# Performance work log

Hardware: AMD Instinct MI355X
Metric: run time of the kernel (lower is better)

## Reference

```python
import jax, jax.numpy as jnp
import numpy as np

N = 262144        # BS(16) * MAX_FRAMES(256) * num_joints(64), flattened
D_IN = 4          # IN_FEAT: (x, y, z, conf) per joint
D_OUT = 512       # OUT_FEAT
NUM_JOINTS = 64   # embedding vocab size
PAD_FRAC = 0.1


def _uniform(key, shape, fan_in):
    s = 1.0 / np.sqrt(fan_in)
    return jax.random.uniform(key, shape, jnp.float32, minval=-s, maxval=s)


def setup_inputs() -> dict:
    key = jax.random.key(0)
    ks = jax.random.split(key, 12)
    joint_info = jax.random.normal(ks[0], (N, D_IN), jnp.float32)
    pad = jax.random.uniform(ks[1], (N,)) < PAD_FRAC
    joint_info = jnp.where(pad[:, None], 0.0, joint_info)  # all-zero rows = padding
    joint_token = jax.random.randint(ks[2], (N,), 0, NUM_JOINTS)
    emb = jax.random.normal(ks[3], (NUM_JOINTS, D_OUT), jnp.float32)
    W1 = _uniform(ks[4], (D_OUT // 4, D_IN), D_IN)
    b1 = _uniform(ks[5], (D_OUT // 4,), D_IN)
    W2 = _uniform(ks[6], (D_OUT // 2, D_OUT // 4), D_OUT // 4)
    b2 = _uniform(ks[7], (D_OUT // 2,), D_OUT // 4)
    W3 = _uniform(ks[8], (D_OUT // 4, D_OUT // 2), D_OUT // 2)
    b3 = _uniform(ks[9], (D_OUT // 4,), D_OUT // 2)
    W4 = _uniform(ks[10], (D_OUT, D_OUT // 4), D_OUT // 4)  # last layer: no bias
    return {"joint_info": joint_info, "joint_token": joint_token, "emb": emb,
            "W1": W1, "b1": b1, "W2": W2, "b2": b2, "W3": W3, "b3": b3, "W4": W4}


def _mlp(x, layers):
    # residual when in/out widths match; GELU (exact, like torch nn.GELU) except after last layer
    out = x
    n = len(layers)
    for i, (W, b) in enumerate(layers):
        y = out @ W.T
        if b is not None:
            y = y + b
        out = y + out if y.shape[-1] == out.shape[-1] else y
        if i != n - 1:
            out = jax.nn.gelu(out, approximate=False)
    return out


def reference(joint_info, joint_token, emb, W1, b1, W2, b2, W3, b3, W4):
    layers = [(W1, b1), (W2, b2), (W3, b3), (W4, None)]
    out = _mlp(joint_info, layers)                 # [N, D_OUT]
    out = out + emb[joint_token]                   # embedding add for non-pad path
    pad_mask = jnp.all(joint_info == 0, axis=-1)   # [N]
    # pad rows get embedding(0); non-pad rows get MLP output + token embedding
    return jnp.where(pad_mask[:, None], emb[0], out)
```

## Files before the change

kernel.cpp:

```cpp
#include <hip/hip_runtime.h>
#include <math.h>


typedef float  f32x4  __attribute__((ext_vector_type(4)));
typedef short  s16x8  __attribute__((ext_vector_type(8)));
typedef __bf16 bf16x8 __attribute__((ext_vector_type(8)));

__device__ __forceinline__ unsigned short f2bf(float x) {
  unsigned u = __builtin_bit_cast(unsigned, x);
  u = (u + 0x7FFFu + ((u >> 16) & 1u)) >> 16;
  return (unsigned short)u;
}
__device__ __forceinline__ float gelu_exact(float x) {
  return 0.5f * x * (1.0f + erff(x * 0.70710678118654752f));
}

__global__ void embed_prep(const float* __restrict__ W2, const float* __restrict__ W3,
                           const float* __restrict__ W4, short* __restrict__ ws) {
  int tid = blockIdx.x * 256 + threadIdx.x;
  const float* W; int K; int base; int e;
  if (tid < 4096)      { W = W2; K = 128; base = 0;     e = tid; }
  else if (tid < 8192) { W = W3; K = 256; base = 32768; e = tid - 4096; }
  else                 { W = W4; K = 128; base = 65536; e = tid - 8192; }
  int lane = e & 63, f = e >> 6;
  int kt = K >> 5;
  int nn = f / kt, kk = f - nn * kt;
  int n  = nn * 16 + (lane & 15);
  int k0 = kk * 32 + (lane >> 4) * 8;
  const float* src = W + n * K + k0;
  s16x8 v;
#pragma unroll
  for (int j = 0; j < 8; j++) v[j] = (short)f2bf(src[j]);
  *reinterpret_cast<s16x8*>(ws + base + e * 8) = v;
}

__global__ __launch_bounds__(256) void embed_main(
    const float* __restrict__ jinfo, const int* __restrict__ jtok,
    const float* __restrict__ emb,   const float* __restrict__ W1,
    const float* __restrict__ b1,    const float* __restrict__ b2,
    const float* __restrict__ b3,    const short* __restrict__ wsW,
    float* __restrict__ out) {
  __shared__ short lds_act[4][8192];
  const int lane = threadIdx.x & 63;
  const int wave = threadIdx.x >> 6;
  const int q = lane >> 4, c = lane & 15;
  const int rowBase = blockIdx.x * 128 + wave * 32;
  short* S = lds_act[wave];

  const float4* jp = reinterpret_cast<const float4*>(jinfo);

  float4 x0 = jp[rowBase + c];
  float4 x1 = jp[rowBase + 16 + c];
  s16x8 a2s[2][4];
#pragma unroll
  for (int kk = 0; kk < 4; kk++) {
#pragma unroll
    for (int j = 0; j < 8; j++) {
      int f = kk * 32 + q * 8 + j;
      float4 w = reinterpret_cast<const float4*>(W1)[f];
      float bb = b1[f];
      float h0 = fmaf(w.x, x0.x, fmaf(w.y, x0.y, fmaf(w.z, x0.z, fmaf(w.w, x0.w, bb))));
      float h1 = fmaf(w.x, x1.x, fmaf(w.y, x1.y, fmaf(w.z, x1.z, fmaf(w.w, x1.w, bb))));
      a2s[0][kk][j] = (short)f2bf(gelu_exact(h0));
      a2s[1][kk][j] = (short)f2bf(gelu_exact(h1));
    }
  }

  const s16x8* fr2 = reinterpret_cast<const s16x8*>(wsW);
  const s16x8* fr3 = reinterpret_cast<const s16x8*>(wsW + 32768);
  const s16x8* fr4 = reinterpret_cast<const s16x8*>(wsW + 65536);

#pragma unroll
  for (int nn = 0; nn < 16; nn++) {
    f32x4 ac0 = {0.f, 0.f, 0.f, 0.f}, ac1 = {0.f, 0.f, 0.f, 0.f};
#pragma unroll
    for (int kk = 0; kk < 4; kk++) {
      bf16x8 bfr = __builtin_bit_cast(bf16x8, fr2[(nn * 4 + kk) * 64 + lane]);
      ac0 = __builtin_amdgcn_mfma_f32_16x16x32_bf16(__builtin_bit_cast(bf16x8, a2s[0][kk]), bfr, ac0, 0, 0, 0);
      ac1 = __builtin_amdgcn_mfma_f32_16x16x32_bf16(__builtin_bit_cast(bf16x8, a2s[1][kk]), bfr, ac1, 0, 0, 0);
    }
    int col = nn * 16 + c;
    float bias = b2[col];
#pragma unroll
    for (int t = 0; t < 2; t++) {
      f32x4 av = t ? ac1 : ac0;
#pragma unroll
      for (int r = 0; r < 4; r++) {
        int m = t * 16 + q * 4 + r;
        S[m * 256 + ((((col >> 3) ^ m) & 31) << 3) + (col & 7)] =
            (short)f2bf(gelu_exact(av[r] + bias));
      }
    }
  }
  __syncthreads();

  s16x8 a3s[2][8];
#pragma unroll
  for (int t = 0; t < 2; t++) {
#pragma unroll
    for (int kk = 0; kk < 8; kk++) {
      int m = t * 16 + c;
      int b = kk * 4 + q;
      a3s[t][kk] = *reinterpret_cast<const s16x8*>(&S[m * 256 + (((b ^ m) & 31) << 3)]);
    }
  }
#pragma unroll
  for (int nn = 0; nn < 8; nn++) {
    f32x4 ac0 = {0.f, 0.f, 0.f, 0.f}, ac1 = {0.f, 0.f, 0.f, 0.f};
#pragma unroll
    for (int kk = 0; kk < 8; kk++) {
      bf16x8 bfr = __builtin_bit_cast(bf16x8, fr3[(nn * 8 + kk) * 64 + lane]);
      ac0 = __builtin_amdgcn_mfma_f32_16x16x32_bf16(__builtin_bit_cast(bf16x8, a3s[0][kk]), bfr, ac0, 0, 0, 0);
      ac1 = __builtin_amdgcn_mfma_f32_16x16x32_bf16(__builtin_bit_cast(bf16x8, a3s[1][kk]), bfr, ac1, 0, 0, 0);
    }
    int col = nn * 16 + c;
    float bias = b3[col];
#pragma unroll
    for (int t = 0; t < 2; t++) {
      f32x4 av = t ? ac1 : ac0;
#pragma unroll
      for (int r = 0; r < 4; r++) {
        int m = t * 16 + q * 4 + r;
        S[m * 256 + ((((col >> 3) ^ m) & 31) << 3) + (col & 7)] =
            (short)f2bf(gelu_exact(av[r] + bias));
      }
    }
  }
  __syncthreads();

  s16x8 a4s[2][4];
#pragma unroll
  for (int t = 0; t < 2; t++) {
#pragma unroll
    for (int kk = 0; kk < 4; kk++) {
      int m = t * 16 + c;
      int b = kk * 4 + q;
      a4s[t][kk] = *reinterpret_cast<const s16x8*>(&S[m * 256 + (((b ^ m) & 31) << 3)]);
    }
  }

  int   offE[8];
  float mul[8];
#pragma unroll
  for (int i = 0; i < 8; i++) {
    int t = i >> 2, r = i & 3;
    int row = rowBase + t * 16 + q * 4 + r;
    float4 x = jp[row];
    bool pad = (x.x == 0.f) && (x.y == 0.f) && (x.z == 0.f) && (x.w == 0.f);
    int tok = jtok[row];
    offE[i] = (pad ? 0 : tok) * 512;
    mul[i]  = pad ? 0.f : 1.f;
  }

#pragma unroll
  for (int nn = 0; nn < 32; nn++) {
    f32x4 ac0 = {0.f, 0.f, 0.f, 0.f}, ac1 = {0.f, 0.f, 0.f, 0.f};
#pragma unroll
    for (int kk = 0; kk < 4; kk++) {
      bf16x8 bfr = __builtin_bit_cast(bf16x8, fr4[(nn * 4 + kk) * 64 + lane]);
      ac0 = __builtin_amdgcn_mfma_f32_16x16x32_bf16(__builtin_bit_cast(bf16x8, a4s[0][kk]), bfr, ac0, 0, 0, 0);
      ac1 = __builtin_amdgcn_mfma_f32_16x16x32_bf16(__builtin_bit_cast(bf16x8, a4s[1][kk]), bfr, ac1, 0, 0, 0);
    }
    int col = nn * 16 + c;
#pragma unroll
    for (int t = 0; t < 2; t++) {
      f32x4 av = t ? ac1 : ac0;
#pragma unroll
      for (int r = 0; r < 4; r++) {
        int i = t * 4 + r;
        int row = rowBase + t * 16 + q * 4 + r;
        out[row * 512 + col] = av[r] * mul[i] + emb[offE[i] + col];
      }
    }
  }
}

extern "C" void kernel_launch(void* const* d_in, const int* in_sizes, int n_in,
                              void* d_out, int out_size, void* d_ws, size_t ws_size,
                              hipStream_t stream) {
  const float* jinfo = (const float*)d_in[0];
  const int*   jtok  = (const int*)d_in[1];
  const float* emb   = (const float*)d_in[2];
  const float* W1    = (const float*)d_in[3];
  const float* b1    = (const float*)d_in[4];
  const float* W2    = (const float*)d_in[5];
  const float* b2    = (const float*)d_in[6];
  const float* W3    = (const float*)d_in[7];
  const float* b3    = (const float*)d_in[8];
  const float* W4    = (const float*)d_in[9];
  float* out = (float*)d_out;
  short* ws  = (short*)d_ws;

  int rows = in_sizes[0] / 4;
  embed_prep<<<64, 256, 0, stream>>>(W2, W3, W4, ws);
  embed_main<<<rows / 128, 256, 0, stream>>>(jinfo, jtok, emb, W1, b1, b2, b3, ws, out);
}
```

Baseline: 929.9 us.

## Split layer-2/3 K-loop to halve LDS, stage layer-4 output for vectorized stores

Layers 2 and 3 are now computed in two halves: each 128-column chunk of the layer-2 activation goes to a half-size LDS buffer and is immediately used as a K-slice for layer 3 accumulation. This halves LDS per block, targeting higher occupancy (launch bounds now request 4 blocks). The final layer writes 64-column tiles through swizzled LDS so each lane emits coalesced float4 stores with float4 embedding loads, instead of scattered scalar stores. Block syncs become wave barriers because each wave owns its LDS slice. The cost is more register pressure from the layer-3 accumulators and extra LDS round trips in the epilogue.

```diff
diff --git a/kernel.cpp b/kernel.cpp
--- a/kernel.cpp
+++ b/kernel.cpp
@@ -14,6 +14,7 @@
 __device__ __forceinline__ float gelu_exact(float x) {
   return 0.5f * x * (1.0f + erff(x * 0.70710678118654752f));
 }
+#define WAVE_FENCE() __builtin_amdgcn_wave_barrier()
 
 __global__ void embed_prep(const float* __restrict__ W2, const float* __restrict__ W3,
                            const float* __restrict__ W4, short* __restrict__ ws) {
@@ -34,18 +35,19 @@
   *reinterpret_cast<s16x8*>(ws + base + e * 8) = v;
 }
 
-__global__ __launch_bounds__(256) void embed_main(
+__global__ __launch_bounds__(256, 4) void embed_main(
     const float* __restrict__ jinfo, const int* __restrict__ jtok,
     const float* __restrict__ emb,   const float* __restrict__ W1,
     const float* __restrict__ b1,    const float* __restrict__ b2,
     const float* __restrict__ b3,    const short* __restrict__ wsW,
     float* __restrict__ out) {
-  __shared__ short lds_act[4][8192];
+  __shared__ short lds_raw[4][4096];
   const int lane = threadIdx.x & 63;
   const int wave = threadIdx.x >> 6;
   const int q = lane >> 4, c = lane & 15;
   const int rowBase = blockIdx.x * 128 + wave * 32;
-  short* S = lds_act[wave];
+  short* S  = lds_raw[wave];
+  float* SF = reinterpret_cast<float*>(S);
 
   const float4* jp = reinterpret_cast<const float4*>(jinfo);
 
@@ -70,81 +72,85 @@
   const s16x8* fr3 = reinterpret_cast<const s16x8*>(wsW + 32768);
   const s16x8* fr4 = reinterpret_cast<const s16x8*>(wsW + 65536);
 
-#pragma unroll
-  for (int nn = 0; nn < 16; nn++) {
-    f32x4 ac0 = {0.f, 0.f, 0.f, 0.f}, ac1 = {0.f, 0.f, 0.f, 0.f};
-#pragma unroll
-    for (int kk = 0; kk < 4; kk++) {
-      bf16x8 bfr = __builtin_bit_cast(bf16x8, fr2[(nn * 4 + kk) * 64 + lane]);
-      ac0 = __builtin_amdgcn_mfma_f32_16x16x32_bf16(__builtin_bit_cast(bf16x8, a2s[0][kk]), bfr, ac0, 0, 0, 0);
-      ac1 = __builtin_amdgcn_mfma_f32_16x16x32_bf16(__builtin_bit_cast(bf16x8, a2s[1][kk]), bfr, ac1, 0, 0, 0);
-    }
-    int col = nn * 16 + c;
-    float bias = b2[col];
-#pragma unroll
-    for (int t = 0; t < 2; t++) {
-      f32x4 av = t ? ac1 : ac0;
+  f32x4 acc3[2][8];
+#pragma unroll
+  for (int t = 0; t < 2; t++)
+#pragma unroll
+    for (int nn = 0; nn < 8; nn++) acc3[t][nn] = (f32x4){0.f, 0.f, 0.f, 0.f};
+
+  for (int h = 0; h < 2; h++) {
+#pragma unroll
+    for (int nn8 = 0; nn8 < 8; nn8++) {
+      f32x4 ac0 = {0.f, 0.f, 0.f, 0.f}, ac1 = {0.f, 0.f, 0.f, 0.f};
+#pragma unroll
+      for (int kk = 0; kk < 4; kk++) {
+        bf16x8 bfr = __builtin_bit_cast(bf16x8, fr2[((h * 8 + nn8) * 4 + kk) * 64 + lane]);
+        ac0 = __builtin_amdgcn_mfma_f32_16x16x32_bf16(__builtin_bit_cast(bf16x8, a2s[0][kk]), bfr, ac0, 0, 0, 0);
+        ac1 = __builtin_amdgcn_mfma_f32_16x16x32_bf16(__builtin_bit_cast(bf16x8, a2s[1][kk]), bfr, ac1, 0, 0, 0);
+      }
+      float bias = b2[(h * 8 + nn8) * 16 + c];
+      int g = nn8 * 2 + (c >> 3), w = c & 7;
+#pragma unroll
+      for (int t = 0; t < 2; t++) {
+        f32x4 av = t ? ac1 : ac0;
+#pragma unroll
+        for (int r = 0; r < 4; r++) {
+          int m = t * 16 + q * 4 + r;
+          S[m * 128 + (((g ^ m) & 15) << 3) + w] = (short)f2bf(gelu_exact(av[r] + bias));
+        }
+      }
+    }
+    WAVE_FENCE();
+    s16x8 a3[2][4];
+#pragma unroll
+    for (int t = 0; t < 2; t++)
+#pragma unroll
+      for (int kkl = 0; kkl < 4; kkl++) {
+        int m = t * 16 + c;
+        int g = kkl * 4 + q;
+        a3[t][kkl] = *reinterpret_cast<const s16x8*>(&S[m * 128 + (((g ^ m) & 15) << 3)]);
+      }
+    WAVE_FENCE();
+#pragma unroll
+    for (int nn = 0; nn < 8; nn++)
+#pragma unroll
+      for (int kkl = 0; kkl < 4; kkl++) {
+        bf16x8 bfr = __builtin_bit_cast(bf16x8, fr3[(nn * 8 + h * 4 + kkl) * 64 + lane]);
+        acc3[0][nn] = __builtin_amdgcn_mfma_f32_16x16x32_bf16(__builtin_bit_cast(bf16x8, a3[0][kkl]), bfr, acc3[0][nn], 0, 0, 0);
+        acc3[1][nn] = __builtin_amdgcn_mfma_f32_16x16x32_bf16(__builtin_bit_cast(bf16x8, a3[1][kkl]), bfr, acc3[1][nn], 0, 0, 0);
+      }
+    WAVE_FENCE();
+  }
+
+#pragma unroll
+  for (int nn = 0; nn < 8; nn++) {
+    float bias = b3[nn * 16 + c];
+    int g = nn * 2 + (c >> 3), w = c & 7;
+#pragma unroll
+    for (int t = 0; t < 2; t++)
 #pragma unroll
       for (int r = 0; r < 4; r++) {
         int m = t * 16 + q * 4 + r;
-        S[m * 256 + ((((col >> 3) ^ m) & 31) << 3) + (col & 7)] =
-            (short)f2bf(gelu_exact(av[r] + bias));
-      }
-    }
-  }
-  __syncthreads();
-
-  s16x8 a3s[2][8];
-#pragma unroll
-  for (int t = 0; t < 2; t++) {
-#pragma unroll
-    for (int kk = 0; kk < 8; kk++) {
-      int m = t * 16 + c;
-      int b = kk * 4 + q;
-      a3s[t][kk] = *reinterpret_cast<const s16x8*>(&S[m * 256 + (((b ^ m) & 31) << 3)]);
-    }
-  }
-#pragma unroll
-  for (int nn = 0; nn < 8; nn++) {
-    f32x4 ac0 = {0.f, 0.f, 0.f, 0.f}, ac1 = {0.f, 0.f, 0.f, 0.f};
-#pragma unroll
-    for (int kk = 0; kk < 8; kk++) {
-      bf16x8 bfr = __builtin_bit_cast(bf16x8, fr3[(nn * 8 + kk) * 64 + lane]);
-      ac0 = __builtin_amdgcn_mfma_f32_16x16x32_bf16(__builtin_bit_cast(bf16x8, a3s[0][kk]), bfr, ac0, 0, 0, 0);
-      ac1 = __builtin_amdgcn_mfma_f32_16x16x32_bf16(__builtin_bit_cast(bf16x8, a3s[1][kk]), bfr, ac1, 0, 0, 0);
-    }
-    int col = nn * 16 + c;
-    float bias = b3[col];
-#pragma unroll
-    for (int t = 0; t < 2; t++) {
-      f32x4 av = t ? ac1 : ac0;
-#pragma unroll
-      for (int r = 0; r < 4; r++) {
-        int m = t * 16 + q * 4 + r;
-        S[m * 256 + ((((col >> 3) ^ m) & 31) << 3) + (col & 7)] =
-            (short)f2bf(gelu_exact(av[r] + bias));
-      }
-    }
-  }
-  __syncthreads();
-
-  s16x8 a4s[2][4];
-#pragma unroll
-  for (int t = 0; t < 2; t++) {
+        S[m * 128 + (((g ^ m) & 15) << 3) + w] = (short)f2bf(gelu_exact(acc3[t][nn][r] + bias));
+      }
+  }
+  WAVE_FENCE();
+  s16x8 a4[2][4];
+#pragma unroll
+  for (int t = 0; t < 2; t++)
 #pragma unroll
     for (int kk = 0; kk < 4; kk++) {
       int m = t * 16 + c;
-      int b = kk * 4 + q;
-      a4s[t][kk] = *reinterpret_cast<const s16x8*>(&S[m * 256 + (((b ^ m) & 31) << 3)]);
-    }
-  }
+      int g = kk * 4 + q;
+      a4[t][kk] = *reinterpret_cast<const s16x8*>(&S[m * 128 + (((g ^ m) & 15) << 3)]);
+    }
+  WAVE_FENCE();
 
   int   offE[8];
   float mul[8];
 #pragma unroll
   for (int i = 0; i < 8; i++) {
-    int t = i >> 2, r = i & 3;
-    int row = rowBase + t * 16 + q * 4 + r;
+    int row = rowBase + 4 * i + (lane >> 4);
     float4 x = jp[row];
     bool pad = (x.x == 0.f) && (x.y == 0.f) && (x.z == 0.f) && (x.w == 0.f);
     int tok = jtok[row];
@@ -153,25 +159,50 @@
   }
 
 #pragma unroll
-  for (int nn = 0; nn < 32; nn++) {
-    f32x4 ac0 = {0.f, 0.f, 0.f, 0.f}, ac1 = {0.f, 0.f, 0.f, 0.f};
-#pragma unroll
-    for (int kk = 0; kk < 4; kk++) {
-      bf16x8 bfr = __builtin_bit_cast(bf16x8, fr4[(nn * 4 + kk) * 64 + lane]);
-      ac0 = __builtin_amdgcn_mfma_f32_16x16x32_bf16(__builtin_bit_cast(bf16x8, a4s[0][kk]), bfr, ac0, 0, 0, 0);
-      ac1 = __builtin_amdgcn_mfma_f32_16x16x32_bf16(__builtin_bit_cast(bf16x8, a4s[1][kk]), bfr, ac1, 0, 0, 0);
-    }
-    int col = nn * 16 + c;
-#pragma unroll
-    for (int t = 0; t < 2; t++) {
-      f32x4 av = t ? ac1 : ac0;
-#pragma unroll
-      for (int r = 0; r < 4; r++) {
-        int i = t * 4 + r;
-        int row = rowBase + t * 16 + q * 4 + r;
-        out[row * 512 + col] = av[r] * mul[i] + emb[offE[i] + col];
-      }
-    }
+  for (int g4 = 0; g4 < 8; g4++) {
+    f32x4 acc4[2][4];
+#pragma unroll
+    for (int t = 0; t < 2; t++)
+#pragma unroll
+      for (int n2 = 0; n2 < 4; n2++) acc4[t][n2] = (f32x4){0.f, 0.f, 0.f, 0.f};
+#pragma unroll
+    for (int n2 = 0; n2 < 4; n2++)
+#pragma unroll
+      for (int kk = 0; kk < 4; kk++) {
+        bf16x8 bfr = __builtin_bit_cast(bf16x8, fr4[((g4 * 4 + n2) * 4 + kk) * 64 + lane]);
+        acc4[0][n2] = __builtin_amdgcn_mfma_f32_16x16x32_bf16(__builtin_bit_cast(bf16x8, a4[0][kk]), bfr, acc4[0][n2], 0, 0, 0);
+        acc4[1][n2] = __builtin_amdgcn_mfma_f32_16x16x32_bf16(__builtin_bit_cast(bf16x8, a4[1][kk]), bfr, acc4[1][n2], 0, 0, 0);
+      }
+    WAVE_FENCE();
+#pragma unroll
+    for (int n2 = 0; n2 < 4; n2++) {
+      int colL = n2 * 16 + c;
+      int cg = colL >> 2, cw = colL & 3;
+#pragma unroll
+      for (int t = 0; t < 2; t++)
+#pragma unroll
+        for (int r = 0; r < 4; r++) {
+          int row = t * 16 + q * 4 + r;
+          SF[row * 64 + (((cg ^ row) & 15) << 2) + cw] = acc4[t][n2][r];
+        }
+    }
+    WAVE_FENCE();
+    int c4 = c * 4;
+    int colG = g4 * 64 + c4;
+#pragma unroll
+    for (int i = 0; i < 8; i++) {
+      int rowL = 4 * i + (lane >> 4);
+      f32x4 v = *reinterpret_cast<const f32x4*>(&SF[rowL * 64 + ((((c4 >> 2) ^ rowL) & 15) << 2)]);
+      float4 e = *reinterpret_cast<const float4*>(emb + offE[i] + colG);
+      float mm = mul[i];
+      float4 res;
+      res.x = fmaf(v[0], mm, e.x);
+      res.y = fmaf(v[1], mm, e.y);
+      res.z = fmaf(v[2], mm, e.z);
+      res.w = fmaf(v[3], mm, e.w);
+      *reinterpret_cast<float4*>(out + (rowBase + rowL) * 512 + colG) = res;
+    }
+    WAVE_FENCE();
   }
 }
 
```

After: 1.228 ms. +32.1%, slower.
